# Optimization experiments

Measured on AMD Instinct MI355X. Metric: run time of the kernel, lower is better.

The kernel has to match this reference:

```python
import jax, jax.numpy as jnp
import numpy as np

G, VPG, CPG, LPC = 32, 512, 1024, 3
N_VARS, N_CLAUSES = G * VPG, G * CPG
N_LITS = N_CLAUSES * LPC
FM, QM, ROUNDS = 128, 32, 4
EPS_NORM, EPS_LOG, EPS_SQRT = 1e-6, 1e-8, 1e-6


def _dense_init(key, fin, fout):
    w = jax.random.normal(key, (fin, fout), jnp.float32) * np.float32(np.sqrt(2.0 / (fin + fout)))
    return w, jnp.zeros((fout,), jnp.float32)


def setup_inputs():
    rng = np.random.default_rng(0)
    g_of_clause = np.repeat(np.arange(G), CPG)
    lit_clause = np.repeat(np.arange(N_CLAUSES), LPC).astype(np.int32)
    # each clause picks LPC variables from its own graph's variable block
    lit_var = (np.repeat(g_of_clause * VPG, LPC) + rng.integers(0, VPG, N_LITS)).astype(np.int32)
    lit_sign = (rng.integers(0, 2, N_LITS) * 2 - 1).astype(np.int32)  # +/-1 literal polarity
    variables_mask = np.repeat(np.arange(G), VPG).astype(np.int32)
    clauses_mask = g_of_clause.astype(np.int32)
    keys = jax.random.split(jax.random.key(0), 13)
    inp = dict(
        lit_var=jnp.asarray(lit_var), lit_sign=jnp.asarray(lit_sign), lit_clause=jnp.asarray(lit_clause),
        variables_mask=jnp.asarray(variables_mask), clauses_mask=jnp.asarray(clauses_mask),
        noise=jax.random.normal(keys[12], (ROUNDS, N_VARS, 4), jnp.float32),
    )
    dims = dict(vq=(FM + 4, 2 * QM, QM), cm=(FM + QM, 3 * FM, FM + QM), ug=(FM + 3 * QM, 2 * FM, FM), vo=(FM, FM, 1))
    ki = 0
    for name, (fin, hid, fout) in dims.items():
        for i, (a, b) in enumerate([(fin, hid), (hid, hid), (hid, fout)]):
            w, bb = _dense_init(keys[ki], a, b); ki += 1
            inp[f'{name}_w{i}'] = w
            inp[f'{name}_b{i}'] = bb
    return inp


def _mlp(x, ps):
    # repo MLP: (layer_count-1) hidden Dense with leaky_relu(0.2), linear output, no layer norm
    for w, b in ps[:-1]:
        x = jax.nn.leaky_relu(x @ w + b, negative_slope=0.2)
    w, b = ps[-1]
    return x @ w + b


def _zero_state(n, f):
    # one_hot(0) - 1/f, scaled by sqrt(f)*0.25
    oh = jnp.zeros((n, f), jnp.float32).at[:, 0].set(1.0)
    return (oh - 1.0 / f) * np.float32(np.sqrt(f) * 0.25)


def _forward(lit_var, lit_sign, lit_clause, variables_mask, clauses_mask, noise, params, checkpoint=False):
    p = list(params)
    vq = [(p[0], p[1]), (p[2], p[3]), (p[4], p[5])]
    cm = [(p[6], p[7]), (p[8], p[9]), (p[10], p[11])]
    ug = [(p[12], p[13]), (p[14], p[15]), (p[16], p[17])]
    vo = [(p[18], p[19]), (p[20], p[21]), (p[22], p[23])]
    seg_sum = jax.ops.segment_sum
    sgn = lit_sign.astype(jnp.float32)[:, None]          # [L,1] +/-1
    pos = (sgn > 0).astype(jnp.float32)
    neg = 1.0 - pos
    var_cnt = seg_sum(jnp.ones((N_VARS,), jnp.float32), variables_mask, G)
    cls_cnt = seg_sum(jnp.ones((N_CLAUSES,), jnp.float32), clauses_mask, G)

    def pair_norm(x, seg, cnt):
        mean = seg_sum(x, seg, G) / cnt[:, None]
        x = x - mean[seg]
        return x * jax.lax.rsqrt(jnp.mean(jnp.square(x), axis=-1, keepdims=True) + EPS_NORM)

    def clause_val(q):
        # softplus_loss: V_c = exp(-sum_{lit in c} softplus(sign * q[var]))  -> [N_CLAUSES, d]
        lit = jax.nn.softplus(q[lit_var] * sgn)
        return jnp.exp(-seg_sum(lit, lit_clause, N_CLAUSES))

    def body(carry, noise_t):
        variables, clause_state = carry
        v1 = jnp.concatenate([variables, noise_t], axis=-1)          # [V, FM+4]
        query = _mlp(v1, vq)                                          # [V, QM]

        def q_loss(q):
            cl = clause_val(q)
            return jnp.sum(cl), cl
        variables_grad, clauses_loss = jax.grad(q_loss, has_aux=True)(query)

        clause_data = _mlp(jnp.concatenate([clause_state, clauses_loss], axis=-1), cm)  # [C, FM+QM]
        vloss = clause_data[:, :QM]
        new_cv = pair_norm(clause_data[:, QM:], clauses_mask, cls_cnt) * 0.25
        clause_state = new_cv + 0.1 * clause_state

        contrib = vloss[lit_clause]                                   # [L, QM]
        loss_pos = seg_sum(contrib * pos, lit_var, N_VARS)            # A_pos @ vloss
        loss_neg = seg_sum(contrib * neg, lit_var, N_VARS)            # A_neg @ vloss

        unit = jnp.concatenate([variables, variables_grad, loss_pos, loss_neg], axis=-1)
        new_vars = pair_norm(_mlp(unit, ug), variables_mask, var_cnt) * 0.25
        variables = new_vars + 0.1 * variables

        logits = _mlp(variables, vo)                                  # [V, 1]
        v = clause_val(logits)
        per_clause = v * (-jnp.log(1.0 - v + EPS_LOG))                # softplus_mixed_loss
        per_graph = seg_sum(per_clause, clauses_mask, G)              # [G, 1]
        logit_loss = jnp.sum(jnp.sqrt(per_graph + EPS_SQRT))

        variables = jax.lax.stop_gradient(variables) * 0.2 + variables * 0.8
        clause_state = jax.lax.stop_gradient(clause_state) * 0.2 + clause_state * 0.8
        return (variables, clause_state), (logit_loss, logits)

    if checkpoint:
        body = jax.checkpoint(body)
    init = (_zero_state(N_VARS, FM), _zero_state(N_CLAUSES, FM))
    _, (step_losses, logits_seq) = jax.lax.scan(body, init, noise)
    return logits_seq[-1], jnp.sum(step_losses) / np.float32(ROUNDS)


def reference(lit_var, lit_sign, lit_clause, variables_mask, clauses_mask, noise,
              vq_w0, vq_b0, vq_w1, vq_b1, vq_w2, vq_b2,
              cm_w0, cm_b0, cm_w1, cm_b1, cm_w2, cm_b2,
              ug_w0, ug_b0, ug_w1, ug_b1, ug_w2, ug_b2,
              vo_w0, vo_b0, vo_w1, vo_b1, vo_w2, vo_b2):
    params = (vq_w0, vq_b0, vq_w1, vq_b1, vq_w2, vq_b2,
              cm_w0, cm_b0, cm_w1, cm_b1, cm_w2, cm_b2,
              ug_w0, ug_b0, ug_w1, ug_b1, ug_w2, ug_b2,
              vo_w0, vo_b0, vo_w1, vo_b1, vo_w2, vo_b2)
    return _forward(lit_var, lit_sign, lit_clause, variables_mask, clauses_mask, noise, params)
```

## Files before the change

### kernel.cpp

```cpp
#include <hip/hip_runtime.h>
#include <hip/hip_bf16.h>
#include <math.h>

#define NG     32
#define NVARS  16384
#define NCLS   32768
#define NLITS  98304
#define NROUNDS 4

typedef __attribute__((ext_vector_type(8))) short bf16x8;
typedef __attribute__((ext_vector_type(4))) float f32x4;

#define OFF_VAR    ((size_t)0)
#define OFF_CST    ((size_t)2097152)
#define OFF_XCMB   ((size_t)6291456)
#define OFF_XUGB   ((size_t)9437184)
#define OFF_ABUF   ((size_t)11534336)
#define OFF_BBUF   ((size_t)17825792)
#define OFF_CD     ((size_t)24117248)
#define OFF_Q      ((size_t)30408704)
#define OFF_VLOSS  ((size_t)31981568)
#define OFF_CMEAN  ((size_t)33030144)
#define OFF_VMEAN  ((size_t)33034240)
#define OFF_LOSS   ((size_t)33038336)
#define OFF_CSO    ((size_t)33038340)
#define OFF_CSE    ((size_t)33054725)
#define OFF_CSC    ((size_t)33153029)
#define OFF_WT     ((size_t)33169416)

#define WT_CM0  ((size_t)0)
#define WT_CM1  ((size_t)73728)
#define WT_CM2  ((size_t)221184)
#define WT_UG0  ((size_t)294912)
#define WT_UG1  ((size_t)360448)
#define WT_UG2  ((size_t)425984)
#define WT_VO0  ((size_t)458752)
#define WT_VO1  ((size_t)475136)
#define WT_VQ0  ((size_t)491520)
#define WT_VQ1  ((size_t)501760)
#define WT_VQ2  ((size_t)505856)

__device__ __forceinline__ float softplus_f(float x) {
  return fmaxf(x, 0.f) + log1pf(expf(-fabsf(x)));
}
__device__ __forceinline__ short f2bf(float x) {
  __hip_bfloat16 h = __float2bfloat16(x);
  return *reinterpret_cast<short*>(&h);
}
__device__ __forceinline__ float bf2f(short s) {
  __hip_bfloat16 h = *reinterpret_cast<__hip_bfloat16*>(&s);
  return __bfloat162float(h);
}

__global__ void init_state_kernel(float* __restrict__ var, float* __restrict__ cst,
                                  short* __restrict__ xugb, short* __restrict__ xcmb,
                                  float* __restrict__ loss, int* __restrict__ cnt) {
  int t = blockIdx.x * blockDim.x + threadIdx.x;
  if (t == 0) *loss = 0.f;
  const int main_total = (NVARS + NCLS) * 128;
  if (t < main_total) {
    int row = t >> 7, m = t & 127;
    const float base = 2.82842712474619f;
    float val = ((m == 0) ? (1.f - 1.f / 128.f) : (-1.f / 128.f)) * base;
    if (row < NVARS) {
      var[(size_t)row * 128 + m] = val;
      xugb[(size_t)row * 256 + m] = f2bf(val);
    } else {
      int c = row - NVARS;
      cst[(size_t)c * 128 + m] = val;
      xcmb[(size_t)c * 192 + m] = f2bf(val);
    }
    return;
  }
  int t2 = t - main_total;
  if (t2 < NVARS * 32) {
    int row = t2 >> 5, j = t2 & 31;
    xugb[(size_t)row * 256 + 224 + j] = 0;
    return;
  }
  int t3 = t2 - NVARS * 32;
  if (t3 < NCLS * 32) {
    int row = t3 >> 5, j = t3 & 31;
    xcmb[(size_t)row * 192 + 160 + j] = 0;
    return;
  }
  int t4 = t3 - NCLS * 32;
  if (t4 < NVARS) cnt[t4] = 0;
}

__global__ void csr_count_kernel(const int* __restrict__ lit_var, int* __restrict__ cnt) {
  int l = blockIdx.x * blockDim.x + threadIdx.x;
  if (l >= NLITS) return;
  atomicAdd(&cnt[lit_var[l]], 1);
}

__global__ __launch_bounds__(1024) void csr_scan_kernel(const int* __restrict__ cnt,
                                                        int* __restrict__ cso,
                                                        int* __restrict__ cur) {
  __shared__ int part[1024];
  int t = threadIdx.x;
  int base = t * 16;
  int local[16];
  int s = 0;
  #pragma unroll
  for (int i = 0; i < 16; ++i) { local[i] = cnt[base + i]; s += local[i]; }
  part[t] = s;
  __syncthreads();
  for (int off = 1; off < 1024; off <<= 1) {
    int v = (t >= off) ? part[t - off] : 0;
    __syncthreads();
    part[t] += v;
    __syncthreads();
  }
  int run = part[t] - s;
  #pragma unroll
  for (int i = 0; i < 16; ++i) {
    cso[base + i] = run;
    cur[base + i] = run;
    run += local[i];
  }
  if (t == 1023) cso[NVARS] = run;
}

__global__ void csr_fill_kernel(const int* __restrict__ lit_var, const int* __restrict__ lit_sign,
                                const int* __restrict__ lit_clause,
                                int* __restrict__ cur, int* __restrict__ cse) {
  int l = blockIdx.x * blockDim.x + threadIdx.x;
  if (l >= NLITS) return;
  int v = lit_var[l];
  int pos = atomicAdd(&cur[v], 1);
  cse[pos] = (lit_clause[l] << 1) | (lit_sign[l] > 0 ? 1 : 0);
}

__global__ void convert_all_kernel(
    const float* __restrict__ cm_w0, const float* __restrict__ cm_w1, const float* __restrict__ cm_w2,
    const float* __restrict__ ug_w0, const float* __restrict__ ug_w1, const float* __restrict__ ug_w2,
    const float* __restrict__ vo_w0, const float* __restrict__ vo_w1,
    const float* __restrict__ vq_w0, const float* __restrict__ vq_w1, const float* __restrict__ vq_w2,
    short* __restrict__ wt) {
  int t = blockIdx.x * blockDim.x + threadIdx.x;
  const float* W; int K, N, Kp; size_t base; int idx;
  if      (t < 73728)  { W = cm_w0; K = 160; N = 384; Kp = 192; base = WT_CM0; idx = t; }
  else if (t < 221184) { W = cm_w1; K = 384; N = 384; Kp = 384; base = WT_CM1; idx = t - 73728; }
  else if (t < 294912) { W = cm_w2; K = 384; N = 160; Kp = 384; base = WT_CM2; idx = t - 221184; }
  else if (t < 360448) { W = ug_w0; K = 224; N = 256; Kp = 256; base = WT_UG0; idx = t - 294912; }
  else if (t < 425984) { W = ug_w1; K = 256; N = 256; Kp = 256; base = WT_UG1; idx = t - 360448; }
  else if (t < 458752) { W = ug_w2; K = 256; N = 128; Kp = 256; base = WT_UG2; idx = t - 425984; }
  else if (t < 475136) { W = vo_w0; K = 128; N = 128; Kp = 128; base = WT_VO0; idx = t - 458752; }
  else if (t < 491520) { W = vo_w1; K = 128; N = 128; Kp = 128; base = WT_VO1; idx = t - 475136; }
  else if (t < 501760) { W = vq_w0; K = 132; N = 64;  Kp = 160; base = WT_VQ0; idx = t - 491520; }
  else if (t < 505856) { W = vq_w1; K = 64;  N = 64;  Kp = 64;  base = WT_VQ1; idx = t - 501760; }
  else if (t < 507904) { W = vq_w2; K = 64;  N = 32;  Kp = 64;  base = WT_VQ2; idx = t - 505856; }
  else return;
  int n = idx / Kp, k = idx - n * Kp;
  float v = (k < K && n < N) ? W[(size_t)k * N + n] : 0.f;
  wt[base + idx] = f2bf(v);
}

__global__ __launch_bounds__(256) void fused_vq_kernel(
    const short* __restrict__ xugb, const float* __restrict__ noise,
    const short* __restrict__ w0, const short* __restrict__ w1, const short* __restrict__ w2,
    const float* __restrict__ b0, const float* __restrict__ b1, const float* __restrict__ b2,
    float* __restrict__ Q) {
  __shared__ short A[64 * 160];
  __shared__ short H1[4][16 * 64];
  __shared__ short H2[4][16 * 64];
  const int wid = threadIdx.x >> 6, lane = threadIdx.x & 63;
  const int rbase = blockIdx.x * 64 + wid * 16;
  #pragma unroll
  for (int i = 0; i < 4; ++i) {
    int s = i * 64 + lane;
    int row = s >> 4, c8 = s & 15;
    *(bf16x8*)&A[(wid * 16 + row) * 160 + c8 * 8] =
        *(const bf16x8*)&xugb[(size_t)(rbase + row) * 256 + c8 * 8];
  }
  {
    int row = lane >> 2, seg = lane & 3;
    bf16x8 z = {0, 0, 0, 0, 0, 0, 0, 0};
    if (seg == 0) {
      float4 nz = *(const float4*)&noise[(size_t)(rbase + row) * 4];
      z[0] = f2bf(nz.x); z[1] = f2bf(nz.y); z[2] = f2bf(nz.z); z[3] = f2bf(nz.w);
    }
    *(bf16x8*)&A[(wid * 16 + row) * 160 + 128 + seg * 8] = z;
  }
  const int kof = (lane >> 4) * 8;
  const int l15 = lane & 15;
  f32x4 acc[4] = {};
  #pragma unroll
  for (int ks = 0; ks < 5; ++ks) {
    bf16x8 a = *(const bf16x8*)&A[(wid * 16 + l15) * 160 + ks * 32 + kof];
    #pragma unroll
    for (int ni = 0; ni < 4; ++ni) {
      bf16x8 b = *(const bf16x8*)&w0[(ni * 16 + l15) * 160 + ks * 32 + kof];
      acc[ni] = __builtin_amdgcn_mfma_f32_16x16x32_bf16(a, b, acc[ni], 0, 0, 0);
    }
  }
  #pragma unroll
  for (int ni = 0; ni < 4; ++ni) {
    int col = ni * 16 + l15;
    float bb = b0[col];
    #pragma unroll
    for (int j = 0; j < 4; ++j) {
      float v = acc[ni][j] + bb; v = v > 0.f ? v : 0.2f * v;
      H1[wid][((lane >> 4) * 4 + j) * 64 + col] = f2bf(v);
    }
  }
  f32x4 acc2[4] = {};
  #pragma unroll
  for (int ks = 0; ks < 2; ++ks) {
    bf16x8 a = *(const bf16x8*)&H1[wid][l15 * 64 + ks * 32 + kof];
    #pragma unroll
    for (int ni = 0; ni < 4; ++ni) {
      bf16x8 b = *(const bf16x8*)&w1[(ni * 16 + l15) * 64 + ks * 32 + kof];
      acc2[ni] = __builtin_amdgcn_mfma_f32_16x16x32_bf16(a, b, acc2[ni], 0, 0, 0);
    }
  }
  #pragma unroll
  for (int ni = 0; ni < 4; ++ni) {
    int col = ni * 16 + l15;
    float bb = b1[col];
    #pragma unroll
    for (int j = 0; j < 4; ++j) {
      float v = acc2[ni][j] + bb; v = v > 0.f ? v : 0.2f * v;
      H2[wid][((lane >> 4) * 4 + j) * 64 + col] = f2bf(v);
    }
  }
  f32x4 acc3[2] = {};
  #pragma unroll
  for (int ks = 0; ks < 2; ++ks) {
    bf16x8 a = *(const bf16x8*)&H2[wid][l15 * 64 + ks * 32 + kof];
    #pragma unroll
    for (int ni = 0; ni < 2; ++ni) {
      bf16x8 b = *(const bf16x8*)&w2[(ni * 16 + l15) * 64 + ks * 32 + kof];
      acc3[ni] = __builtin_amdgcn_mfma_f32_16x16x32_bf16(a, b, acc3[ni], 0, 0, 0);
    }
  }
  #pragma unroll
  for (int ni = 0; ni < 2; ++ni) {
    int col = ni * 16 + l15;
    float bb = b2[col];
    #pragma unroll
    for (int j = 0; j < 4; ++j)
      Q[(size_t)(rbase + (lane >> 4) * 4 + j) * 32 + col] = acc3[ni][j] + bb;
  }
}

__global__ void fused_clause_kernel(const float* __restrict__ Q, const int* __restrict__ lit_var,
                                    const int* __restrict__ lit_sign,
                                    short* __restrict__ xcmb, float* __restrict__ meanz) {
  int t = blockIdx.x * blockDim.x + threadIdx.x;
  if (t < 2 * 32 * 128) meanz[t] = 0.f;
  if (t >= NCLS * 32) return;
  int c = t >> 5, m = t & 31;
  int l0 = 3 * c;
  int v0 = lit_var[l0], v1 = lit_var[l0 + 1], v2 = lit_var[l0 + 2];
  int s0 = lit_sign[l0], s1 = lit_sign[l0 + 1], s2 = lit_sign[l0 + 2];
  float q0 = Q[(size_t)v0 * 32 + m];
  float q1 = Q[(size_t)v1 * 32 + m];
  float q2 = Q[(size_t)v2 * 32 + m];
  float sp = softplus_f(q0 * (float)s0) + softplus_f(q1 * (float)s1) + softplus_f(q2 * (float)s2);
  float cl = expf(-sp);
  xcmb[(size_t)c * 192 + 128 + m] = f2bf(cl);
}

template<int TN, bool RELU, bool OUTBF16, int EPI>
__global__ __launch_bounds__(256) void gemm_mfma_kernel(
    const short* __restrict__ A, int lda,
    const short* __restrict__ Wt,
    const float* __restrict__ bias, int nbias,
    void* __restrict__ Cout, int Np, int Kp,
    short* __restrict__ aux,
    float* __restrict__ meanbuf, float inv_cnt, int gshift) {
  constexpr int NB = TN / 32;
  __shared__ short As[128 * 64];
  __shared__ short Bs[TN * 64];
  const int bn = blockIdx.x * TN;
  const int bm = blockIdx.y * 128;
  const int tid  = threadIdx.x;
  const int wid  = tid >> 6;
  const int lane = tid & 63;
  const int wm = (wid >> 1) * 64;
  const int wn = (wid & 1) * (TN / 2);

  f32x4 acc[4][NB] = {};

  for (int k0 = 0; k0 < Kp; k0 += 64) {
    #pragma unroll
    for (int i = 0; i < 4; ++i) {
      int s = (i * 4 + wid) * 64 + lane;
      int row = s >> 3, cs = (s & 7) << 3;
      const short* src = A + (size_t)(bm + row) * lda + k0 + cs;
      __builtin_amdgcn_global_load_lds(
          (const __attribute__((address_space(1))) void*)src,
          (__attribute__((address_space(3))) void*)(As + (size_t)(i * 4 + wid) * 64 * 8),
          16, 0, 0);
    }
    #pragma unroll
    for (int i = 0; i < TN / 32; ++i) {
      int s = (i * 4 + wid) * 64 + lane;
      int n = s >> 3, cs = (s & 7) << 3;
      const short* src = Wt + (size_t)(bn + n) * Kp + k0 + cs;
      __builtin_amdgcn_global_load_lds(
          (const __attribute__((address_space(1))) void*)src,
          (__attribute__((address_space(3))) void*)(Bs + (size_t)(i * 4 + wid) * 64 * 8),
          16, 0, 0);
    }
    __syncthreads();

    #pragma unroll
    for (int ks = 0; ks < 2; ++ks) {
      const int kof = ks * 32 + (lane >> 4) * 8;
      bf16x8 a[4], b[NB];
      #pragma unroll
      for (int mi = 0; mi < 4; ++mi)
        a[mi] = *(const bf16x8*)&As[(wm + mi * 16 + (lane & 15)) * 64 + kof];
      #pragma unroll
      for (int ni = 0; ni < NB; ++ni)
        b[ni] = *(const bf16x8*)&Bs[(wn + ni * 16 + (lane & 15)) * 64 + kof];
      #pragma unroll
      for (int mi = 0; mi < 4; ++mi)
        #pragma unroll
        for (int ni = 0; ni < NB; ++ni)
          acc[mi][ni] = __builtin_amdgcn_mfma_f32_16x16x32_bf16(a[mi], b[ni], acc[mi][ni], 0, 0, 0);
    }
    __syncthreads();
  }

  const int col0 = bn + wn + (lane & 15);
  const int row0 = bm + wm + (lane >> 4) * 4;
  #pragma unroll
  for (int ni = 0; ni < NB; ++ni) {
    int col = col0 + ni * 16;
    float bv = (col < nbias) ? bias[col] : 0.f;
    float colsum = 0.f;
    #pragma unroll
    for (int mi = 0; mi < 4; ++mi) {
      #pragma unroll
      for (int j = 0; j < 4; ++j) {
        int row = row0 + mi * 16 + j;
        float v = acc[mi][ni][j] + bv;
        if (EPI == 0) {
          if (RELU) v = v > 0.f ? v : 0.2f * v;
          if (OUTBF16) ((short*)Cout)[(size_t)row * Np + col] = f2bf(v);
          else         ((float*)Cout)[(size_t)row * Np + col] = v;
        } else if (EPI == 1) {
          if (col < 32) {
            aux[(size_t)row * 32 + col] = f2bf(v);
          } else if (col < 160) {
            ((short*)Cout)[(size_t)row * Np + col] = f2bf(v);
            colsum += v;
          }
        } else {
          ((short*)Cout)[(size_t)row * Np + col] = f2bf(v);
          colsum += v;
        }
      }
    }
    if ((EPI == 1 && col >= 32 && col < 160) || EPI == 2) {
      colsum += __shfl_xor(colsum, 16);
      colsum += __shfl_xor(colsum, 32);
      if ((lane >> 4) == 0) {
        int midx = (EPI == 1) ? (col - 32) : col;
        atomicAdd(&meanbuf[(size_t)(bm >> gshift) * 128 + midx], colsum * inv_cnt);
      }
    }
  }
}

__global__ __launch_bounds__(256) void pnc_gather_kernel(
    const short* __restrict__ CDb, const float* __restrict__ cmean,
    float* __restrict__ cst, short* __restrict__ xcmb,
    const float* __restrict__ Q, const int* __restrict__ cso, const int* __restrict__ cse,
    const short* __restrict__ vloss, short* __restrict__ xugb) {
  int b = blockIdx.x;
  if (b < NCLS / 4) {
    int wid = threadIdx.x >> 6;
    int lane = threadIdx.x & 63;
    int row = b * 4 + wid;
    int g = row >> 10;
    const short* xp = CDb + (size_t)row * 192 + 32;
    float y0 = bf2f(xp[lane])      - cmean[g * 128 + lane];
    float y1 = bf2f(xp[lane + 64]) - cmean[g * 128 + lane + 64];
    float ss = y0 * y0 + y1 * y1;
    #pragma unroll
    for (int o = 32; o > 0; o >>= 1) ss += __shfl_xor(ss, o);
    float inv = rsqrtf(ss * (1.f / 128.f) + 1e-6f);
    float* sp = cst + (size_t)row * 128;
    float s0 = y0 * inv * 0.25f + 0.1f * sp[lane];
    float s1 = y1 * inv * 0.25f + 0.1f * sp[lane + 64];
    sp[lane]      = s0;
    sp[lane + 64] = s1;
    xcmb[(size_t)row * 192 + lane]      = f2bf(s0);
    xcmb[(size_t)row * 192 + lane + 64] = f2bf(s1);
  } else {
    int t = (b - NCLS / 4) * 256 + threadIdx.x;
    int v = t >> 5, m = t & 31;
    float q = Q[(size_t)v * 32 + m];
    float sig = 1.f / (1.f + expf(-q));
    float vgs = 0.f, lps = 0.f, lns = 0.f;
    int e0 = cso[v], e1 = cso[v + 1];
    for (int e = e0; e < e1; ++e) {
      int ent = cse[e];
      int c = ent >> 1;
      bool pos = ent & 1;
      float clc = bf2f(xcmb[(size_t)c * 192 + 128 + m]);
      vgs -= clc * (sig - (pos ? 0.f : 1.f));
      float vl = bf2f(vloss[(size_t)c * 32 + m]);
      if (pos) lps += vl; else lns += vl;
    }
    short* xp = xugb + (size_t)v * 256 + 128;
    xp[m]      = f2bf(vgs);
    xp[32 + m] = f2bf(lps);
    xp[64 + m] = f2bf(lns);
  }
}

__global__ __launch_bounds__(256) void pairnorm_update_kernel(
    const short* __restrict__ x, int stride, int coloff,
    const float* __restrict__ mean, float* __restrict__ state,
    short* __restrict__ bout, int bstride, int rows_per_g) {
  int wid = threadIdx.x >> 6;
  int lane = threadIdx.x & 63;
  int row = blockIdx.x * 4 + wid;
  int g = row / rows_per_g;
  const short* xp = x + (size_t)row * stride + coloff;
  float y0 = bf2f(xp[lane])      - mean[g * 128 + lane];
  float y1 = bf2f(xp[lane + 64]) - mean[g * 128 + lane + 64];
  float ss = y0 * y0 + y1 * y1;
  #pragma unroll
  for (int o = 32; o > 0; o >>= 1) ss += __shfl_xor(ss, o);
  float inv = rsqrtf(ss * (1.f / 128.f) + 1e-6f);
  float* sp = state + (size_t)row * 128;
  float s0 = y0 * inv * 0.25f + 0.1f * sp[lane];
  float s1 = y1 * inv * 0.25f + 0.1f * sp[lane + 64];
  sp[lane]      = s0;
  sp[lane + 64] = s1;
  bout[(size_t)row * bstride + lane]      = f2bf(s0);
  bout[(size_t)row * bstride + lane + 64] = f2bf(s1);
}

__global__ __launch_bounds__(256) void fused_vo_kernel(
    const short* __restrict__ xugb,
    const short* __restrict__ w0, const short* __restrict__ w1,
    const float* __restrict__ b0, const float* __restrict__ b1,
    const float* __restrict__ w2, const float* __restrict__ b2,
    float* __restrict__ logits) {
  __shared__ short A[64 * 128];
  __shared__ short H1[4][16 * 128];
  __shared__ short H2[4][16 * 128];
  const int wid = threadIdx.x >> 6, lane = threadIdx.x & 63;
  const int rbase = blockIdx.x * 64 + wid * 16;
  #pragma unroll
  for (int i = 0; i < 4; ++i) {
    int s = i * 64 + lane;
    int row = s >> 4, c8 = s & 15;
    *(bf16x8*)&A[(wid * 16 + row) * 128 + c8 * 8] =
        *(const bf16x8*)&xugb[(size_t)(rbase + row) * 256 + c8 * 8];
  }
  const int kof = (lane >> 4) * 8;
  const int l15 = lane & 15;
  f32x4 acc[8] = {};
  #pragma unroll
  for (int ks = 0; ks < 4; ++ks) {
    bf16x8 a = *(const bf16x8*)&A[(wid * 16 + l15) * 128 + ks * 32 + kof];
    #pragma unroll
    for (int ni = 0; ni < 8; ++ni) {
      bf16x8 b = *(const bf16x8*)&w0[(ni * 16 + l15) * 128 + ks * 32 + kof];
      acc[ni] = __builtin_amdgcn_mfma_f32_16x16x32_bf16(a, b, acc[ni], 0, 0, 0);
    }
  }
  #pragma unroll
  for (int ni = 0; ni < 8; ++ni) {
    int col = ni * 16 + l15;
    float bb = b0[col];
    #pragma unroll
    for (int j = 0; j < 4; ++j) {
      float v = acc[ni][j] + bb; v = v > 0.f ? v : 0.2f * v;
      H1[wid][((lane >> 4) * 4 + j) * 128 + col] = f2bf(v);
    }
  }
  f32x4 acc2[8] = {};
  #pragma unroll
  for (int ks = 0; ks < 4; ++ks) {
    bf16x8 a = *(const bf16x8*)&H1[wid][l15 * 128 + ks * 32 + kof];
    #pragma unroll
    for (int ni = 0; ni < 8; ++ni) {
      bf16x8 b = *(const bf16x8*)&w1[(ni * 16 + l15) * 128 + ks * 32 + kof];
      acc2[ni] = __builtin_amdgcn_mfma_f32_16x16x32_bf16(a, b, acc2[ni], 0, 0, 0);
    }
  }
  #pragma unroll
  for (int ni = 0; ni < 8; ++ni) {
    int col = ni * 16 + l15;
    float bb = b1[col];
    #pragma unroll
    for (int j = 0; j < 4; ++j) {
      float v = acc2[ni][j] + bb; v = v > 0.f ? v : 0.2f * v;
      H2[wid][((lane >> 4) * 4 + j) * 128 + col] = f2bf(v);
    }
  }
  {
    int row = lane >> 2, q = lane & 3;
    float s = 0.f;
    #pragma unroll
    for (int jj = 0; jj < 4; ++jj) {
      bf16x8 h = *(const bf16x8*)&H2[wid][row * 128 + q * 32 + jj * 8];
      #pragma unroll
      for (int e = 0; e < 8; ++e) s += bf2f(h[e]) * w2[q * 32 + jj * 8 + e];
    }
    s += __shfl_xor(s, 1);
    s += __shfl_xor(s, 2);
    if (q == 0) logits[rbase + row] = s + b2[0];
  }
}

__global__ __launch_bounds__(1024) void fused_loss_kernel(
    const float* __restrict__ logits, const int* __restrict__ lit_var,
    const int* __restrict__ lit_sign, float* __restrict__ loss) {
  __shared__ float lg[512];
  __shared__ float red[16];
  int g = blockIdx.x, tid = threadIdx.x;
  if (tid < 512) lg[tid] = logits[(size_t)g * 512 + tid];
  __syncthreads();
  int c = g * 1024 + tid;
  float s = 0.f;
  #pragma unroll
  for (int i = 0; i < 3; ++i) {
    int l = 3 * c + i;
    float sg = (float)lit_sign[l];
    s += softplus_f(lg[lit_var[l] - g * 512] * sg);
  }
  float vv = expf(-s);
  float pcv = vv * (-logf(1.f - vv + 1e-8f));
  #pragma unroll
  for (int o = 32; o > 0; o >>= 1) pcv += __shfl_xor(pcv, o);
  if ((tid & 63) == 0) red[tid >> 6] = pcv;
  __syncthreads();
  if (tid < 16) {
    float x = red[tid];
    #pragma unroll
    for (int o = 8; o > 0; o >>= 1) x += __shfl_xor(x, o);
    if (tid == 0) atomicAdd(loss, sqrtf(x + 1e-6f));
  }
}

__global__ void finalize_kernel(const float* __restrict__ loss_acc, float* __restrict__ out) {
  out[0] = loss_acc[0] * 0.25f;
}

extern "C" void kernel_launch(void* const* d_in, const int* in_sizes, int n_in,
                              void* d_out, int out_size, void* d_ws, size_t ws_size,
                              hipStream_t stream) {
  const int* lit_var    = (const int*)d_in[0];
  const int* lit_sign   = (const int*)d_in[1];
  const int* lit_clause = (const int*)d_in[2];
  const float* noise    = (const float*)d_in[5];
  const float* vq_w0 = (const float*)d_in[6];   const float* vq_b0 = (const float*)d_in[7];
  const float* vq_w1 = (const float*)d_in[8];   const float* vq_b1 = (const float*)d_in[9];
  const float* vq_w2 = (const float*)d_in[10];  const float* vq_b2 = (const float*)d_in[11];
  const float* cm_w0 = (const float*)d_in[12];  const float* cm_b0 = (const float*)d_in[13];
  const float* cm_w1 = (const float*)d_in[14];  const float* cm_b1 = (const float*)d_in[15];
  const float* cm_w2 = (const float*)d_in[16];  const float* cm_b2 = (const float*)d_in[17];
  const float* ug_w0 = (const float*)d_in[18];  const float* ug_b0 = (const float*)d_in[19];
  const float* ug_w1 = (const float*)d_in[20];  const float* ug_b1 = (const float*)d_in[21];
  const float* ug_w2 = (const float*)d_in[22];  const float* ug_b2 = (const float*)d_in[23];
  const float* vo_w0 = (const float*)d_in[24];  const float* vo_b0 = (const float*)d_in[25];
  const float* vo_w1 = (const float*)d_in[26];  const float* vo_b1 = (const float*)d_in[27];
  const float* vo_w2 = (const float*)d_in[28];  const float* vo_b2 = (const float*)d_in[29];

  float* ws = (float*)d_ws;
  float* var   = ws + OFF_VAR;
  float* cst   = ws + OFF_CST;
  short* xcmb  = (short*)(ws + OFF_XCMB);
  short* xugb  = (short*)(ws + OFF_XUGB);
  short* bufA  = (short*)(ws + OFF_ABUF);
  short* bufB  = (short*)(ws + OFF_BBUF);
  short* CDb   = (short*)(ws + OFF_CD);
  float* Q     = ws + OFF_Q;
  short* vloss = (short*)(ws + OFF_VLOSS);
  float* cmean = ws + OFF_CMEAN;
  float* vmean = ws + OFF_VMEAN;
  float* loss  = ws + OFF_LOSS;
  int*   cso   = (int*)(ws + OFF_CSO);
  int*   cse   = (int*)(ws + OFF_CSE);
  int*   csc   = (int*)(ws + OFF_CSC);
  short* wt    = (short*)(ws + OFF_WT);
  float* logits = (float*)d_out;
  float* loss_out = (float*)d_out + NVARS;

  convert_all_kernel<<<1984, 256, 0, stream>>>(cm_w0, cm_w1, cm_w2, ug_w0, ug_w1, ug_w2,
                                               vo_w0, vo_w1, vq_w0, vq_w1, vq_w2, wt);
  init_state_kernel<<<30784, 256, 0, stream>>>(var, cst, xugb, xcmb, loss, csc);
  csr_count_kernel<<<NLITS / 256, 256, 0, stream>>>(lit_var, csc);
  csr_scan_kernel<<<1, 1024, 0, stream>>>(csc, cso, csc);
  csr_fill_kernel<<<NLITS / 256, 256, 0, stream>>>(lit_var, lit_sign, lit_clause, csc, cse);

  for (int r = 0; r < NROUNDS; ++r) {
    const float* noise_r = noise + (size_t)r * NVARS * 4;

    fused_vq_kernel<<<NVARS / 64, 256, 0, stream>>>(
        xugb, noise_r, wt + WT_VQ0, wt + WT_VQ1, wt + WT_VQ2, vq_b0, vq_b1, vq_b2, Q);

    fused_clause_kernel<<<NCLS * 32 / 256, 256, 0, stream>>>(Q, lit_var, lit_sign, xcmb, cmean);

    gemm_mfma_kernel<128, true, true, 0><<<dim3(3, NCLS / 128), 256, 0, stream>>>(
        xcmb, 192, wt + WT_CM0, cm_b0, 384, bufA, 384, 192, nullptr, nullptr, 0.f, 0);
    gemm_mfma_kernel<128, true, true, 0><<<dim3(3, NCLS / 128), 256, 0, stream>>>(
        bufA, 384, wt + WT_CM1, cm_b1, 384, bufB, 384, 384, nullptr, nullptr, 0.f, 0);
    gemm_mfma_kernel<64, false, false, 1><<<dim3(3, NCLS / 128), 256, 0, stream>>>(
        bufB, 384, wt + WT_CM2, cm_b2, 160, CDb, 192, 384, vloss, cmean, 1.f / 1024.f, 10);

    pnc_gather_kernel<<<NCLS / 4 + NVARS * 32 / 256, 256, 0, stream>>>(
        CDb, cmean, cst, xcmb, Q, cso, cse, vloss, xugb);

    gemm_mfma_kernel<128, true, true, 0><<<dim3(2, NVARS / 128), 256, 0, stream>>>(
        xugb, 256, wt + WT_UG0, ug_b0, 256, bufA, 256, 256, nullptr, nullptr, 0.f, 0);
    gemm_mfma_kernel<128, true, true, 0><<<dim3(2, NVARS / 128), 256, 0, stream>>>(
        bufA, 256, wt + WT_UG1, ug_b1, 256, bufB, 256, 256, nullptr, nullptr, 0.f, 0);
    gemm_mfma_kernel<64, false, false, 2><<<dim3(2, NVARS / 128), 256, 0, stream>>>(
        bufB, 256, wt + WT_UG2, ug_b2, 128, CDb, 128, 256, nullptr, vmean, 1.f / 512.f, 9);

    pairnorm_update_kernel<<<NVARS / 4, 256, 0, stream>>>(CDb, 128, 0, vmean, var, xugb, 256, 512);

    fused_vo_kernel<<<NVARS / 64, 256, 0, stream>>>(
        xugb, wt + WT_VO0, wt + WT_VO1, vo_b0, vo_b1, vo_w2, vo_b2, logits);

    fused_loss_kernel<<<NG, 1024, 0, stream>>>(logits, lit_var, lit_sign, loss);
  }

  finalize_kernel<<<1, 1, 0, stream>>>(loss, loss_out);
}
```

Baseline: 672.2 us.

## Fuse clause MLP layers 0-1 and update-gate MLP into single kernels

Adds fused_cm01_kernel, which runs the first two clause-MLP layers per 64-row tile and keeps the hidden activations in LDS. Adds fused_ug012_kernel, which runs all three update-gate MLP layers in one kernel with an atomic per-graph mean epilogue. Together they remove four GEMM launches per round and the global round-trips through the intermediate buffer. The trade-off is that weights are read straight from global memory per MFMA fragment without LDS staging, and the large LDS footprint (about 75 KB for cm01) lowers occupancy.

```diff
diff --git a/kernel.cpp b/kernel.cpp
--- a/kernel.cpp
+++ b/kernel.cpp
@@ -261,6 +261,217 @@
   float sp = softplus_f(q0 * (float)s0) + softplus_f(q1 * (float)s1) + softplus_f(q2 * (float)s2);
   float cl = expf(-sp);
   xcmb[(size_t)c * 192 + 128 + m] = f2bf(cl);
+}
+
+__global__ __launch_bounds__(256) void fused_cm01_kernel(
+    const short* __restrict__ xcmb,
+    const short* __restrict__ w0, const short* __restrict__ w1,
+    const float* __restrict__ b0, const float* __restrict__ b1,
+    short* __restrict__ outB) {
+  __shared__ short Xs[64 * 200];
+  __shared__ short H1s[64 * 392];
+  const int tid = threadIdx.x;
+  const int wid = tid >> 6, lane = tid & 63;
+  const int wr = (wid >> 1) * 32, wc = (wid & 1) * 192;
+  const int rbase = blockIdx.x * 64;
+  const int l15 = lane & 15;
+  const int koff = (lane >> 4) * 8;
+
+  for (int i = 0; i < 6; ++i) {
+    int c = i * 256 + tid;
+    int row = c / 24, c8 = c - row * 24;
+    bf16x8 v = *(const bf16x8*)&xcmb[(size_t)(rbase + row) * 192 + c8 * 8];
+    *(bf16x8*)&Xs[row * 200 + c8 * 8] = v;
+  }
+  __syncthreads();
+
+  {
+    f32x4 acc[2][12] = {};
+    #pragma unroll
+    for (int kf = 0; kf < 6; ++kf) {
+      bf16x8 a[2];
+      #pragma unroll
+      for (int mi = 0; mi < 2; ++mi)
+        a[mi] = *(const bf16x8*)&Xs[(wr + mi * 16 + l15) * 200 + kf * 32 + koff];
+      #pragma unroll
+      for (int nf = 0; nf < 12; ++nf) {
+        bf16x8 b = *(const bf16x8*)&w0[(size_t)(wc + nf * 16 + l15) * 192 + kf * 32 + koff];
+        #pragma unroll
+        for (int mi = 0; mi < 2; ++mi)
+          acc[mi][nf] = __builtin_amdgcn_mfma_f32_16x16x32_bf16(a[mi], b, acc[mi][nf], 0, 0, 0);
+      }
+    }
+    #pragma unroll
+    for (int nf = 0; nf < 12; ++nf) {
+      int col = wc + nf * 16 + l15;
+      float bb = b0[col];
+      #pragma unroll
+      for (int mi = 0; mi < 2; ++mi)
+        #pragma unroll
+        for (int j = 0; j < 4; ++j) {
+          float v = acc[mi][nf][j] + bb; v = v > 0.f ? v : 0.2f * v;
+          H1s[(wr + mi * 16 + (lane >> 4) * 4 + j) * 392 + col] = f2bf(v);
+        }
+    }
+  }
+  __syncthreads();
+
+  {
+    f32x4 acc[2][12] = {};
+    #pragma unroll
+    for (int kf = 0; kf < 12; ++kf) {
+      bf16x8 a[2];
+      #pragma unroll
+      for (int mi = 0; mi < 2; ++mi)
+        a[mi] = *(const bf16x8*)&H1s[(wr + mi * 16 + l15) * 392 + kf * 32 + koff];
+      #pragma unroll
+      for (int nf = 0; nf < 12; ++nf) {
+        bf16x8 b = *(const bf16x8*)&w1[(size_t)(wc + nf * 16 + l15) * 384 + kf * 32 + koff];
+        #pragma unroll
+        for (int mi = 0; mi < 2; ++mi)
+          acc[mi][nf] = __builtin_amdgcn_mfma_f32_16x16x32_bf16(a[mi], b, acc[mi][nf], 0, 0, 0);
+      }
+    }
+    #pragma unroll
+    for (int nf = 0; nf < 12; ++nf) {
+      int col = wc + nf * 16 + l15;
+      float bb = b1[col];
+      #pragma unroll
+      for (int mi = 0; mi < 2; ++mi)
+        #pragma unroll
+        for (int j = 0; j < 4; ++j) {
+          float v = acc[mi][nf][j] + bb; v = v > 0.f ? v : 0.2f * v;
+          int row = rbase + wr + mi * 16 + (lane >> 4) * 4 + j;
+          outB[(size_t)row * 384 + col] = f2bf(v);
+        }
+    }
+  }
+}
+
+__global__ __launch_bounds__(256) void fused_ug012_kernel(
+    const short* __restrict__ xugb,
+    const short* __restrict__ w0, const short* __restrict__ w1, const short* __restrict__ w2,
+    const float* __restrict__ b0, const float* __restrict__ b1, const float* __restrict__ b2,
+    short* __restrict__ outB, float* __restrict__ vmean) {
+  __shared__ short Xs[64 * 264];
+  __shared__ short Hs[64 * 264];
+  const int tid = threadIdx.x;
+  const int wid = tid >> 6, lane = tid & 63;
+  const int wr = (wid >> 1) * 32;
+  const int wcH = (wid & 1) * 128;
+  const int l15 = lane & 15;
+  const int koff = (lane >> 4) * 8;
+  const int rbase = blockIdx.x * 64;
+
+  for (int i = 0; i < 8; ++i) {
+    int c = i * 256 + tid;
+    int row = c >> 5, c8 = c & 31;
+    bf16x8 v = *(const bf16x8*)&xugb[(size_t)(rbase + row) * 256 + c8 * 8];
+    *(bf16x8*)&Xs[row * 264 + c8 * 8] = v;
+  }
+  __syncthreads();
+
+  {
+    f32x4 acc[2][8] = {};
+    #pragma unroll
+    for (int kf = 0; kf < 8; ++kf) {
+      bf16x8 a[2];
+      #pragma unroll
+      for (int mi = 0; mi < 2; ++mi)
+        a[mi] = *(const bf16x8*)&Xs[(wr + mi * 16 + l15) * 264 + kf * 32 + koff];
+      #pragma unroll
+      for (int nf = 0; nf < 8; ++nf) {
+        bf16x8 b = *(const bf16x8*)&w0[(size_t)(wcH + nf * 16 + l15) * 256 + kf * 32 + koff];
+        #pragma unroll
+        for (int mi = 0; mi < 2; ++mi)
+          acc[mi][nf] = __builtin_amdgcn_mfma_f32_16x16x32_bf16(a[mi], b, acc[mi][nf], 0, 0, 0);
+      }
+    }
+    #pragma unroll
+    for (int nf = 0; nf < 8; ++nf) {
+      int col = wcH + nf * 16 + l15;
+      float bb = b0[col];
+      #pragma unroll
+      for (int mi = 0; mi < 2; ++mi)
+        #pragma unroll
+        for (int j = 0; j < 4; ++j) {
+          float v = acc[mi][nf][j] + bb; v = v > 0.f ? v : 0.2f * v;
+          Hs[(wr + mi * 16 + (lane >> 4) * 4 + j) * 264 + col] = f2bf(v);
+        }
+    }
+  }
+  __syncthreads();
+
+  {
+    f32x4 acc[2][8] = {};
+    #pragma unroll
+    for (int kf = 0; kf < 8; ++kf) {
+      bf16x8 a[2];
+      #pragma unroll
+      for (int mi = 0; mi < 2; ++mi)
+        a[mi] = *(const bf16x8*)&Hs[(wr + mi * 16 + l15) * 264 + kf * 32 + koff];
+      #pragma unroll
+      for (int nf = 0; nf < 8; ++nf) {
+        bf16x8 b = *(const bf16x8*)&w1[(size_t)(wcH + nf * 16 + l15) * 256 + kf * 32 + koff];
+        #pragma unroll
+        for (int mi = 0; mi < 2; ++mi)
+          acc[mi][nf] = __builtin_amdgcn_mfma_f32_16x16x32_bf16(a[mi], b, acc[mi][nf], 0, 0, 0);
+      }
+    }
+    __syncthreads();
+    #pragma unroll
+    for (int nf = 0; nf < 8; ++nf) {
+      int col = wcH + nf * 16 + l15;
+      float bb = b1[col];
+      #pragma unroll
+      for (int mi = 0; mi < 2; ++mi)
+        #pragma unroll
+        for (int j = 0; j < 4; ++j) {
+          float v = acc[mi][nf][j] + bb; v = v > 0.f ? v : 0.2f * v;
+          Xs[(wr + mi * 16 + (lane >> 4) * 4 + j) * 264 + col] = f2bf(v);
+        }
+    }
+  }
+  __syncthreads();
+
+  {
+    const int wcO = (wid & 1) * 64;
+    f32x4 acc[2][4] = {};
+    #pragma unroll
+    for (int kf = 0; kf < 8; ++kf) {
+      bf16x8 a[2];
+      #pragma unroll
+      for (int mi = 0; mi < 2; ++mi)
+        a[mi] = *(const bf16x8*)&Xs[(wr + mi * 16 + l15) * 264 + kf * 32 + koff];
+      #pragma unroll
+      for (int nf = 0; nf < 4; ++nf) {
+        bf16x8 b = *(const bf16x8*)&w2[(size_t)(wcO + nf * 16 + l15) * 256 + kf * 32 + koff];
+        #pragma unroll
+        for (int mi = 0; mi < 2; ++mi)
+          acc[mi][nf] = __builtin_amdgcn_mfma_f32_16x16x32_bf16(a[mi], b, acc[mi][nf], 0, 0, 0);
+      }
+    }
+    int g = rbase >> 9;
+    #pragma unroll
+    for (int nf = 0; nf < 4; ++nf) {
+      int col = wcO + nf * 16 + l15;
+      float bb = b2[col];
+      float colsum = 0.f;
+      #pragma unroll
+      for (int mi = 0; mi < 2; ++mi)
+        #pragma unroll
+        for (int j = 0; j < 4; ++j) {
+          float v = acc[mi][nf][j] + bb;
+          int row = rbase + wr + mi * 16 + (lane >> 4) * 4 + j;
+          outB[(size_t)row * 128 + col] = f2bf(v);
+          colsum += v;
+        }
+      colsum += __shfl_xor(colsum, 16);
+      colsum += __shfl_xor(colsum, 32);
+      if ((lane >> 4) == 0)
+        atomicAdd(&vmean[(size_t)g * 128 + col], colsum * (1.f / 512.f));
+    }
+  }
 }
 
 template<int TN, bool RELU, bool OUTBF16, int EPI>
@@ -573,7 +784,6 @@
   float* cst   = ws + OFF_CST;
   short* xcmb  = (short*)(ws + OFF_XCMB);
   short* xugb  = (short*)(ws + OFF_XUGB);
-  short* bufA  = (short*)(ws + OFF_ABUF);
   short* bufB  = (short*)(ws + OFF_BBUF);
   short* CDb   = (short*)(ws + OFF_CD);
   float* Q     = ws + OFF_Q;
@@ -603,22 +813,17 @@
 
     fused_clause_kernel<<<NCLS * 32 / 256, 256, 0, stream>>>(Q, lit_var, lit_sign, xcmb, cmean);
 
-    gemm_mfma_kernel<128, true, true, 0><<<dim3(3, NCLS / 128), 256, 0, stream>>>(
-        xcmb, 192, wt + WT_CM0, cm_b0, 384, bufA, 384, 192, nullptr, nullptr, 0.f, 0);
-    gemm_mfma_kernel<128, true, true, 0><<<dim3(3, NCLS / 128), 256, 0, stream>>>(
-        bufA, 384, wt + WT_CM1, cm_b1, 384, bufB, 384, 384, nullptr, nullptr, 0.f, 0);
+    fused_cm01_kernel<<<NCLS / 64, 256, 0, stream>>>(
+        xcmb, wt + WT_CM0, wt + WT_CM1, cm_b0, cm_b1, bufB);
+
     gemm_mfma_kernel<64, false, false, 1><<<dim3(3, NCLS / 128), 256, 0, stream>>>(
         bufB, 384, wt + WT_CM2, cm_b2, 160, CDb, 192, 384, vloss, cmean, 1.f / 1024.f, 10);
 
     pnc_gather_kernel<<<NCLS / 4 + NVARS * 32 / 256, 256, 0, stream>>>(
         CDb, cmean, cst, xcmb, Q, cso, cse, vloss, xugb);
 
-    gemm_mfma_kernel<128, true, true, 0><<<dim3(2, NVARS / 128), 256, 0, stream>>>(
-        xugb, 256, wt + WT_UG0, ug_b0, 256, bufA, 256, 256, nullptr, nullptr, 0.f, 0);
-    gemm_mfma_kernel<128, true, true, 0><<<dim3(2, NVARS / 128), 256, 0, stream>>>(
-        bufA, 256, wt + WT_UG1, ug_b1, 256, bufB, 256, 256, nullptr, nullptr, 0.f, 0);
-    gemm_mfma_kernel<64, false, false, 2><<<dim3(2, NVARS / 128), 256, 0, stream>>>(
-        bufB, 256, wt + WT_UG2, ug_b2, 128, CDb, 128, 256, nullptr, vmean, 1.f / 512.f, 9);
+    fused_ug012_kernel<<<NVARS / 64, 256, 0, stream>>>(
+        xugb, wt + WT_UG0, wt + WT_UG1, wt + WT_UG2, ug_b0, ug_b1, ug_b2, CDb, vmean);
 
     pairnorm_update_kernel<<<NVARS / 4, 256, 0, stream>>>(CDb, 128, 0, vmean, var, xugb, 256, 512);
 
```

After: 756.1 us. +12.5%, slower.

## Drop fp32 state copies and pack clause values with vloss for gathers

Applied to the files above, without the earlier changes.

Removes the fp32 variable and clause state buffers and keeps the recurrent state only in the bf16 GEMM input buffers, reading and updating it in place during pairnorm. The clause values and the per-clause vloss are packed into one 64-wide bf16 array so the variable-side gather touches a single row per clause instead of two scattered buffers. This cuts memory traffic in the pairnorm and gather kernels. The cost is that the residual state is carried in bf16 precision across rounds, which adds rounding error.

```diff
diff --git a/kernel.cpp b/kernel.cpp
--- a/kernel.cpp
+++ b/kernel.cpp
@@ -11,15 +11,13 @@
 typedef __attribute__((ext_vector_type(8))) short bf16x8;
 typedef __attribute__((ext_vector_type(4))) float f32x4;
 
-#define OFF_VAR    ((size_t)0)
-#define OFF_CST    ((size_t)2097152)
+#define OFF_CLVL   ((size_t)0)
 #define OFF_XCMB   ((size_t)6291456)
 #define OFF_XUGB   ((size_t)9437184)
 #define OFF_ABUF   ((size_t)11534336)
 #define OFF_BBUF   ((size_t)17825792)
 #define OFF_CD     ((size_t)24117248)
 #define OFF_Q      ((size_t)30408704)
-#define OFF_VLOSS  ((size_t)31981568)
 #define OFF_CMEAN  ((size_t)33030144)
 #define OFF_VMEAN  ((size_t)33034240)
 #define OFF_LOSS   ((size_t)33038336)
@@ -52,8 +50,7 @@
   return __bfloat162float(h);
 }
 
-__global__ void init_state_kernel(float* __restrict__ var, float* __restrict__ cst,
-                                  short* __restrict__ xugb, short* __restrict__ xcmb,
+__global__ void init_state_kernel(short* __restrict__ xugb, short* __restrict__ xcmb,
                                   float* __restrict__ loss, int* __restrict__ cnt) {
   int t = blockIdx.x * blockDim.x + threadIdx.x;
   if (t == 0) *loss = 0.f;
@@ -62,14 +59,8 @@
     int row = t >> 7, m = t & 127;
     const float base = 2.82842712474619f;
     float val = ((m == 0) ? (1.f - 1.f / 128.f) : (-1.f / 128.f)) * base;
-    if (row < NVARS) {
-      var[(size_t)row * 128 + m] = val;
-      xugb[(size_t)row * 256 + m] = f2bf(val);
-    } else {
-      int c = row - NVARS;
-      cst[(size_t)c * 128 + m] = val;
-      xcmb[(size_t)c * 192 + m] = f2bf(val);
-    }
+    if (row < NVARS) xugb[(size_t)row * 256 + m] = f2bf(val);
+    else             xcmb[(size_t)(row - NVARS) * 192 + m] = f2bf(val);
     return;
   }
   int t2 = t - main_total;
@@ -247,7 +238,8 @@
 
 __global__ void fused_clause_kernel(const float* __restrict__ Q, const int* __restrict__ lit_var,
                                     const int* __restrict__ lit_sign,
-                                    short* __restrict__ xcmb, float* __restrict__ meanz) {
+                                    short* __restrict__ xcmb, short* __restrict__ clvl,
+                                    float* __restrict__ meanz) {
   int t = blockIdx.x * blockDim.x + threadIdx.x;
   if (t < 2 * 32 * 128) meanz[t] = 0.f;
   if (t >= NCLS * 32) return;
@@ -260,7 +252,9 @@
   float q2 = Q[(size_t)v2 * 32 + m];
   float sp = softplus_f(q0 * (float)s0) + softplus_f(q1 * (float)s1) + softplus_f(q2 * (float)s2);
   float cl = expf(-sp);
-  xcmb[(size_t)c * 192 + 128 + m] = f2bf(cl);
+  short clb = f2bf(cl);
+  xcmb[(size_t)c * 192 + 128 + m] = clb;
+  clvl[(size_t)c * 64 + m] = clb;
 }
 
 template<int TN, bool RELU, bool OUTBF16, int EPI>
@@ -345,7 +339,7 @@
           else         ((float*)Cout)[(size_t)row * Np + col] = v;
         } else if (EPI == 1) {
           if (col < 32) {
-            aux[(size_t)row * 32 + col] = f2bf(v);
+            aux[(size_t)row * 64 + 32 + col] = f2bf(v);
           } else if (col < 160) {
             ((short*)Cout)[(size_t)row * Np + col] = f2bf(v);
             colsum += v;
@@ -369,9 +363,9 @@
 
 __global__ __launch_bounds__(256) void pnc_gather_kernel(
     const short* __restrict__ CDb, const float* __restrict__ cmean,
-    float* __restrict__ cst, short* __restrict__ xcmb,
+    short* __restrict__ xcmb,
     const float* __restrict__ Q, const int* __restrict__ cso, const int* __restrict__ cse,
-    const short* __restrict__ vloss, short* __restrict__ xugb) {
+    const short* __restrict__ clvl, short* __restrict__ xugb) {
   int b = blockIdx.x;
   if (b < NCLS / 4) {
     int wid = threadIdx.x >> 6;
@@ -385,13 +379,11 @@
     #pragma unroll
     for (int o = 32; o > 0; o >>= 1) ss += __shfl_xor(ss, o);
     float inv = rsqrtf(ss * (1.f / 128.f) + 1e-6f);
-    float* sp = cst + (size_t)row * 128;
-    float s0 = y0 * inv * 0.25f + 0.1f * sp[lane];
-    float s1 = y1 * inv * 0.25f + 0.1f * sp[lane + 64];
-    sp[lane]      = s0;
-    sp[lane + 64] = s1;
-    xcmb[(size_t)row * 192 + lane]      = f2bf(s0);
-    xcmb[(size_t)row * 192 + lane + 64] = f2bf(s1);
+    short* sp = xcmb + (size_t)row * 192;
+    float s0 = y0 * inv * 0.25f + 0.1f * bf2f(sp[lane]);
+    float s1 = y1 * inv * 0.25f + 0.1f * bf2f(sp[lane + 64]);
+    sp[lane]      = f2bf(s0);
+    sp[lane + 64] = f2bf(s1);
   } else {
     int t = (b - NCLS / 4) * 256 + threadIdx.x;
     int v = t >> 5, m = t & 31;
@@ -403,9 +395,9 @@
       int ent = cse[e];
       int c = ent >> 1;
       bool pos = ent & 1;
-      float clc = bf2f(xcmb[(size_t)c * 192 + 128 + m]);
+      float clc = bf2f(clvl[(size_t)c * 64 + m]);
+      float vl  = bf2f(clvl[(size_t)c * 64 + 32 + m]);
       vgs -= clc * (sig - (pos ? 0.f : 1.f));
-      float vl = bf2f(vloss[(size_t)c * 32 + m]);
       if (pos) lps += vl; else lns += vl;
     }
     short* xp = xugb + (size_t)v * 256 + 128;
@@ -416,27 +408,23 @@
 }
 
 __global__ __launch_bounds__(256) void pairnorm_update_kernel(
-    const short* __restrict__ x, int stride, int coloff,
-    const float* __restrict__ mean, float* __restrict__ state,
-    short* __restrict__ bout, int bstride, int rows_per_g) {
+    const short* __restrict__ CDb, const float* __restrict__ vmean,
+    short* __restrict__ xugb) {
   int wid = threadIdx.x >> 6;
   int lane = threadIdx.x & 63;
   int row = blockIdx.x * 4 + wid;
-  int g = row / rows_per_g;
-  const short* xp = x + (size_t)row * stride + coloff;
-  float y0 = bf2f(xp[lane])      - mean[g * 128 + lane];
-  float y1 = bf2f(xp[lane + 64]) - mean[g * 128 + lane + 64];
+  int g = row >> 9;
+  float y0 = bf2f(CDb[(size_t)row * 128 + lane])      - vmean[g * 128 + lane];
+  float y1 = bf2f(CDb[(size_t)row * 128 + lane + 64]) - vmean[g * 128 + lane + 64];
   float ss = y0 * y0 + y1 * y1;
   #pragma unroll
   for (int o = 32; o > 0; o >>= 1) ss += __shfl_xor(ss, o);
   float inv = rsqrtf(ss * (1.f / 128.f) + 1e-6f);
-  float* sp = state + (size_t)row * 128;
-  float s0 = y0 * inv * 0.25f + 0.1f * sp[lane];
-  float s1 = y1 * inv * 0.25f + 0.1f * sp[lane + 64];
-  sp[lane]      = s0;
-  sp[lane + 64] = s1;
-  bout[(size_t)row * bstride + lane]      = f2bf(s0);
-  bout[(size_t)row * bstride + lane + 64] = f2bf(s1);
+  short* sp = xugb + (size_t)row * 256;
+  float s0 = y0 * inv * 0.25f + 0.1f * bf2f(sp[lane]);
+  float s1 = y1 * inv * 0.25f + 0.1f * bf2f(sp[lane + 64]);
+  sp[lane]      = f2bf(s0);
+  sp[lane + 64] = f2bf(s1);
 }
 
 __global__ __launch_bounds__(256) void fused_vo_kernel(
@@ -569,15 +557,13 @@
   const float* vo_w2 = (const float*)d_in[28];  const float* vo_b2 = (const float*)d_in[29];
 
   float* ws = (float*)d_ws;
-  float* var   = ws + OFF_VAR;
-  float* cst   = ws + OFF_CST;
+  short* clvl  = (short*)(ws + OFF_CLVL);
   short* xcmb  = (short*)(ws + OFF_XCMB);
   short* xugb  = (short*)(ws + OFF_XUGB);
   short* bufA  = (short*)(ws + OFF_ABUF);
   short* bufB  = (short*)(ws + OFF_BBUF);
   short* CDb   = (short*)(ws + OFF_CD);
   float* Q     = ws + OFF_Q;
-  short* vloss = (short*)(ws + OFF_VLOSS);
   float* cmean = ws + OFF_CMEAN;
   float* vmean = ws + OFF_VMEAN;
   float* loss  = ws + OFF_LOSS;
@@ -590,7 +576,7 @@
 
   convert_all_kernel<<<1984, 256, 0, stream>>>(cm_w0, cm_w1, cm_w2, ug_w0, ug_w1, ug_w2,
                                                vo_w0, vo_w1, vq_w0, vq_w1, vq_w2, wt);
-  init_state_kernel<<<30784, 256, 0, stream>>>(var, cst, xugb, xcmb, loss, csc);
+  init_state_kernel<<<30784, 256, 0, stream>>>(xugb, xcmb, loss, csc);
   csr_count_kernel<<<NLITS / 256, 256, 0, stream>>>(lit_var, csc);
   csr_scan_kernel<<<1, 1024, 0, stream>>>(csc, cso, csc);
   csr_fill_kernel<<<NLITS / 256, 256, 0, stream>>>(lit_var, lit_sign, lit_clause, csc, cse);
@@ -601,17 +587,17 @@
     fused_vq_kernel<<<NVARS / 64, 256, 0, stream>>>(
         xugb, noise_r, wt + WT_VQ0, wt + WT_VQ1, wt + WT_VQ2, vq_b0, vq_b1, vq_b2, Q);
 
-    fused_clause_kernel<<<NCLS * 32 / 256, 256, 0, stream>>>(Q, lit_var, lit_sign, xcmb, cmean);
+    fused_clause_kernel<<<NCLS * 32 / 256, 256, 0, stream>>>(Q, lit_var, lit_sign, xcmb, clvl, cmean);
 
     gemm_mfma_kernel<128, true, true, 0><<<dim3(3, NCLS / 128), 256, 0, stream>>>(
         xcmb, 192, wt + WT_CM0, cm_b0, 384, bufA, 384, 192, nullptr, nullptr, 0.f, 0);
     gemm_mfma_kernel<128, true, true, 0><<<dim3(3, NCLS / 128), 256, 0, stream>>>(
         bufA, 384, wt + WT_CM1, cm_b1, 384, bufB, 384, 384, nullptr, nullptr, 0.f, 0);
     gemm_mfma_kernel<64, false, false, 1><<<dim3(3, NCLS / 128), 256, 0, stream>>>(
-        bufB, 384, wt + WT_CM2, cm_b2, 160, CDb, 192, 384, vloss, cmean, 1.f / 1024.f, 10);
+        bufB, 384, wt + WT_CM2, cm_b2, 160, CDb, 192, 384, clvl, cmean, 1.f / 1024.f, 10);
 
     pnc_gather_kernel<<<NCLS / 4 + NVARS * 32 / 256, 256, 0, stream>>>(
-        CDb, cmean, cst, xcmb, Q, cso, cse, vloss, xugb);
+        CDb, cmean, xcmb, Q, cso, cse, clvl, xugb);
 
     gemm_mfma_kernel<128, true, true, 0><<<dim3(2, NVARS / 128), 256, 0, stream>>>(
         xugb, 256, wt + WT_UG0, ug_b0, 256, bufA, 256, 256, nullptr, nullptr, 0.f, 0);
@@ -620,7 +606,7 @@
     gemm_mfma_kernel<64, false, false, 2><<<dim3(2, NVARS / 128), 256, 0, stream>>>(
         bufB, 256, wt + WT_UG2, ug_b2, 128, CDb, 128, 256, nullptr, vmean, 1.f / 512.f, 9);
 
-    pairnorm_update_kernel<<<NVARS / 4, 256, 0, stream>>>(CDb, 128, 0, vmean, var, xugb, 256, 512);
+    pairnorm_update_kernel<<<NVARS / 4, 256, 0, stream>>>(CDb, vmean, xugb);
 
     fused_vo_kernel<<<NVARS / 64, 256, 0, stream>>>(
         xugb, wt + WT_VO0, wt + WT_VO1, vo_b0, vo_b1, vo_w2, vo_b2, logits);
```

After: 654.3 us. -2.7%, faster.
